# Optimization experiments

Hardware: AMD Instinct MI355X
Metric: run time of the kernel (lower is better)

The kernel has to match this reference:

```python
import jax, jax.numpy as jnp
import numpy as np

F, N, C, H, M = 256, 400, 128, 8, 128  # frames, batch*joints, mdl_channels, heads, max_pos
E = C // H


def _layer_norm(z, g, b, eps=1e-5):
    mu = jnp.mean(z, axis=-1, keepdims=True)
    var = jnp.mean((z - mu) ** 2, axis=-1, keepdims=True)
    return (z - mu) * jax.lax.rsqrt(var + eps) * g + b


def setup_inputs() -> dict:
    key = jax.random.key(0)
    ks = jax.random.split(key, 16)
    s = 0.02
    return {
        "x": jax.random.normal(ks[0], (F, N, C), jnp.float32),
        "tree_encoding": jax.random.normal(ks[1], (N, C), jnp.float32),
        "W_qkv": jax.random.normal(ks[2], (3 * C, C), jnp.float32) * s,      # Linear weight (out,in), no bias
        "W_tree_k": jax.random.normal(ks[3], (C, C), jnp.float32) * s,
        "W_tree_v": jax.random.normal(ks[4], (C, C), jnp.float32) * s,
        "emb": jax.random.normal(ks[5], (2 * M + 1, E), jnp.float32) * s,    # distance embedding table
        "W_beta": jax.random.normal(ks[6], (1, 3 * C), jnp.float32) * s,     # lin_beta (out,in), no bias
        "ln1_g": jnp.ones((C,), jnp.float32),
        "ln1_b": jnp.zeros((C,), jnp.float32),
        "ln2_g": jnp.ones((C,), jnp.float32),
        "ln2_b": jnp.zeros((C,), jnp.float32),
        "W1": jax.random.normal(ks[7], (C, C), jnp.float32) * s,
        "b1": jnp.zeros((C,), jnp.float32),
        "W2": jax.random.normal(ks[8], (C, C), jnp.float32) * s,
        "b2": jnp.zeros((C,), jnp.float32),
    }


def reference(x, tree_encoding, W_qkv, W_tree_k, W_tree_v, emb, W_beta,
              ln1_g, ln1_b, ln2_g, ln2_b, W1, b1, W2, b2):
    f, n, c = x.shape
    # qkv projection, no bias
    qkv = x @ W_qkv.T                          # (f, n, 3c)
    q, k, v = jnp.split(qkv, 3, axis=-1)       # each (f, n, c)
    # tree positional encoding added to key/value
    k = k + (tree_encoding @ W_tree_k)[None]
    v = v + (tree_encoding @ W_tree_v)[None]
    # (f, n, c) -> (n, f, h, e): n is the attention batch, f is sequence length
    to_heads = lambda t: t.transpose(1, 0, 2).reshape(n, f, H, E)
    qh, kh, vh = to_heads(q), to_heads(k), to_heads(v)
    # content scores
    qk = jnp.einsum('nlhe,nshe->nhls', qh, kh)
    # relative position bias
    ids = jnp.arange(f)
    dist = jnp.clip(ids[:, None] - ids[None, :], -M, M) + M   # (f, f)
    pe = emb[dist]                                            # (f, f, e)
    qk = qk + jnp.einsum('nlhe,lse->nhls', qh, pe)
    qk = qk + jnp.einsum('nshe,lse->nhls', kh, pe)
    scale = 1.0 / (E ** 0.5)
    att = jax.nn.softmax(qk * scale, axis=-1)                 # (n, h, f, f)
    out = jnp.einsum('nhls,nshe->nlhe', att, vh)              # (n, f, h, e)
    y = out.reshape(n, f, c).transpose(1, 0, 2)               # (f, n, c)
    # gated AddNorm (beta=True): x is residual, y is attention output
    gate = jax.nn.sigmoid(jnp.concatenate([y, x, y - x], axis=-1) @ W_beta.T)
    h1 = _layer_norm(gate * x + (1.0 - gate) * y, ln1_g, ln1_b)
    # FFN (GELU exact, as torch nn.GELU default)
    ff = jax.nn.gelu(h1 @ W1.T + b1, approximate=False) @ W2.T + b2
    return _layer_norm(ff + h1, ln2_g, ln2_b)
```

## Files before the change

kernel.cpp:

```cpp
#include <hip/hip_runtime.h>
#include <math.h>

#define F_DIM 256
#define N_DIM 400
#define C_DIM 128
#define H_DIM 8
#define E_DIM 16
#define ROWS  (F_DIM * N_DIM)
#define SBUF  (N_DIM * H_DIM * F_DIM * E_DIM)

#define S_SCALE 0.6005612043932249f

typedef _Float16 half2_t __attribute__((ext_vector_type(2)));
typedef _Float16 f16x8   __attribute__((ext_vector_type(8)));
typedef float    f32x16  __attribute__((ext_vector_type(16)));
typedef float    f32x4   __attribute__((ext_vector_type(4)));

struct H2x4 { half2_t h[4]; };

__device__ inline f16x8 pack8(float4 a, float4 b) {
    H2x4 t;
    t.h[0] = __builtin_bit_cast(half2_t, __builtin_amdgcn_cvt_pkrtz(a.x, a.y));
    t.h[1] = __builtin_bit_cast(half2_t, __builtin_amdgcn_cvt_pkrtz(a.z, a.w));
    t.h[2] = __builtin_bit_cast(half2_t, __builtin_amdgcn_cvt_pkrtz(b.x, b.y));
    t.h[3] = __builtin_bit_cast(half2_t, __builtin_amdgcn_cvt_pkrtz(b.z, b.w));
    return __builtin_bit_cast(f16x8, t);
}

__device__ inline _Float16 h_rtz(float v) {
    half2_t p = __builtin_bit_cast(half2_t, __builtin_amdgcn_cvt_pkrtz(v, v));
    return p[0];
}

__device__ inline int iclamp256(int v) { return v < 0 ? 0 : (v > 256 ? 256 : v); }

__global__ __launch_bounds__(256) void prep_pack(
    const float* __restrict__ x, const float* __restrict__ Wq,
    const float* __restrict__ emb, const float* __restrict__ te,
    const float* __restrict__ Wtk, const float* __restrict__ Wtv,
    _Float16* __restrict__ xh, _Float16* __restrict__ Wqh,
    _Float16* __restrict__ embh, float* __restrict__ tk, float* __restrict__ tv)
{
    int bid = blockIdx.x;
    int t   = threadIdx.x;
    if (bid < 6400) {
        int i = (bid * 256 + t) * 8;
        const float4* s = (const float4*)(x + i);
        *(uint4*)(xh + i) = __builtin_bit_cast(uint4, pack8(s[0], s[1]));
    } else if (bid < 6424) {
        int i = ((bid - 6400) * 256 + t) * 8;
        const float4* s = (const float4*)(Wq + i);
        *(uint4*)(Wqh + i) = __builtin_bit_cast(uint4, pack8(s[0], s[1]));
    } else if (bid < 6426) {
        int r = (bid - 6424) * 256 + t;
        if (r > 256) return;
        const float4* er = (const float4*)(emb + r * 16);
        float4 e0 = er[0], e1 = er[1], e2 = er[2], e3 = er[3];
        e0.x *= S_SCALE; e0.y *= S_SCALE; e0.z *= S_SCALE; e0.w *= S_SCALE;
        e1.x *= S_SCALE; e1.y *= S_SCALE; e1.z *= S_SCALE; e1.w *= S_SCALE;
        e2.x *= S_SCALE; e2.y *= S_SCALE; e2.z *= S_SCALE; e2.w *= S_SCALE;
        e3.x *= S_SCALE; e3.y *= S_SCALE; e3.z *= S_SCALE; e3.w *= S_SCALE;
        *(uint4*)(embh + r * 16)     = __builtin_bit_cast(uint4, pack8(e0, e1));
        *(uint4*)(embh + r * 16 + 8) = __builtin_bit_cast(uint4, pack8(e2, e3));
    } else {
        int n = bid - 6426;
        const float* W = (t < 128) ? Wtk : Wtv;
        float* outp    = (t < 128) ? tk : tv;
        int j = t & 127;
        float acc = 0.f;
        #pragma unroll 4
        for (int c = 0; c < 128; ++c)
            acc += te[n * 128 + c] * W[c * 128 + j];
        outp[n * 128 + j] = acc;
    }
}

__global__ __launch_bounds__(256) void qkv_gemm(
    const _Float16* __restrict__ xh, const _Float16* __restrict__ Wqh,
    const float* __restrict__ tk, const float* __restrict__ tv,
    _Float16* __restrict__ qn, _Float16* __restrict__ kn, _Float16* __restrict__ vn)
{
    int tid  = threadIdx.x;
    int wave = tid >> 6, lane = tid & 63;
    int m32  = lane & 31, khalf = lane >> 5;

    int bid = blockIdx.x;
    int xcd = bid & 7;
    int tt  = bid >> 3;
    int cb  = tt % 6;
    int rp  = (tt / 6) * 8 + xcd;
    int row0 = rp * 64 + (wave & 1) * 32;
    int col0 = cb * 64 + (wave >> 1) * 32;

    const _Float16* xp = xh  + (row0 + m32) * 128 + khalf * 8;
    const _Float16* wp = Wqh + (col0 + m32) * 128 + khalf * 8;

    f32x16 acc;
    #pragma unroll
    for (int i = 0; i < 16; ++i) acc[i] = 0.f;

    #pragma unroll
    for (int k0 = 0; k0 < 128; k0 += 16) {
        f16x8 xa = __builtin_bit_cast(f16x8, *(const uint4*)(xp + k0));
        f16x8 wa = __builtin_bit_cast(f16x8, *(const uint4*)(wp + k0));
        acc = __builtin_amdgcn_mfma_f32_32x32x16_f16(xa, wa, acc, 0, 0, 0);
    }

    int o   = col0 + m32;
    int sec = o >> 7;
    int rem = o & 127;
    #pragma unroll
    for (int reg = 0; reg < 16; ++reg) {
        int r = row0 + (reg & 3) + 8 * (reg >> 2) + 4 * khalf;
        float val = acc[reg];
        if (sec == 0) {
            qn[r * 128 + rem] = h_rtz(val * S_SCALE);
        } else {
            int f = r / 400;
            int n = r - f * 400;
            if (sec == 1) {
                kn[r * 128 + rem] = h_rtz((val + tk[n * 128 + rem]) * S_SCALE);
            } else {
                vn[r * 128 + rem] = (_Float16)(val + tv[n * 128 + rem]);
            }
        }
    }
}

__global__ __launch_bounds__(256) void v_pack(
    const _Float16* __restrict__ vn, _Float16* __restrict__ vT)
{
    __shared__ _Float16 sm[16 * 264];
    int bn = blockIdx.x;
    int n  = bn >> 3, h = bn & 7;
    int t  = threadIdx.x;

    const uint4* src = (const uint4*)(vn + (t * 400 + n) * 128 + h * 16);
    uint4 a = src[0], b = src[1];
    union { uint4 u; _Float16 hv[8]; } ua, ub;
    ua.u = a; ub.u = b;
    #pragma unroll
    for (int e = 0; e < 8; ++e) sm[e * 264 + t]       = ua.hv[e];
    #pragma unroll
    for (int e = 0; e < 8; ++e) sm[(e + 8) * 264 + t] = ub.hv[e];
    __syncthreads();

    #pragma unroll
    for (int k = 0; k < 2; ++k) {
        int idx = (k * 256 + t) * 8;
        int e = idx >> 8, f0 = idx & 255;
        uint4 o = *(const uint4*)(sm + e * 264 + f0);
        *(uint4*)(vT + bn * 4096 + idx) = o;
    }
}

#define R2_STRIDE 258
#define PS_STRIDE 40

__global__ __launch_bounds__(512, 4) void attn_kernel(
    const _Float16* __restrict__ qb, const _Float16* __restrict__ kb,
    const _Float16* __restrict__ vb, const _Float16* __restrict__ embh,
    _Float16* __restrict__ y)
{
    __shared__ __align__(16) _Float16 R2sh[32 * R2_STRIDE];
    __shared__ __align__(16) _Float16 Psh[8 * 32 * PS_STRIDE];

    int tid  = threadIdx.x;
    int wave = tid >> 6, lane = tid & 63;
    int bid  = blockIdx.x;
    int bn   = (bid & 7) * 400 + (bid >> 3);
    int n    = bn >> 3, h = bn & 7;
    int base = bn * 4096;

    int nn  = lane & 31;
    int kh  = lane >> 5;
    int khb = (lane & 32) << 2;
    int cbase = 31 + 4 * kh - nn;
    int dbase = 4 * kh - nn;
    int q16 = (lane >> 4) & 3;

    int nat_off = n * 128 + h * 16 + kh * 8;

    f16x8 aq = __builtin_bit_cast(f16x8,
        *(const uint4*)(qb + (32 * wave + nn) * 51200 + nat_off));

    f16x8 bones;
    #pragma unroll
    for (int i = 0; i < 8; ++i) bones[i] = (_Float16)1.0f;

    f32x4 O[2];
    f32x4 Od[2];
    #pragma unroll
    for (int a = 0; a < 2; ++a)
        #pragma unroll
        for (int r = 0; r < 4; ++r) { O[a][r] = 0.f; Od[a][r] = 0.f; }

    _Float16* psw = Psh + wave * 32 * PS_STRIDE;

    for (int st = 0; st < 8; ++st) {
        f16x8 bk = __builtin_bit_cast(f16x8,
            *(const uint4*)(kb + (32 * st + nn) * 51200 + nat_off));

        auto r2tile = [&](int ct) {
            int erow = 32 * ct + nn; if (erow > 256) erow = 256;
            f16x8 be = __builtin_bit_cast(f16x8,
                *(const uint4*)(embh + erow * 16 + kh * 8));
            f32x16 c2;
            #pragma unroll
            for (int i = 0; i < 16; ++i) c2[i] = 0.f;
            c2 = __builtin_amdgcn_mfma_f32_32x32x16_f16(bk, be, c2, 0, 0, 0);
            int col = 32 * ct + nn;
            if (col <= 256) {
                #pragma unroll
                for (int r = 0; r < 16; ++r) {
                    int srow = (r & 3) + 8 * (r >> 2) + 4 * kh;
                    R2sh[srow * R2_STRIDE + col] = (_Float16)c2[r];
                }
            }
        };
        r2tile(wave);
        if (wave == (st & 7)) r2tile(8);
        __syncthreads();

        f16x8 bv = __builtin_bit_cast(f16x8,
            *(const uint4*)(vb + base + (lane & 15) * 256 + 32 * st + q16 * 8));

        int U0 = 32 * wave - 32 * st + 128;

        f32x16 S;
        #pragma unroll
        for (int i = 0; i < 16; ++i) S[i] = 0.f;
        S = __builtin_amdgcn_mfma_f32_32x32x16_f16(aq, bk, S, 0, 0, 0);

        int br0 = iclamp256(U0 - 31 + nn);
        int br1 = iclamp256(U0 + 1 + nn);
        f16x8 be0 = __builtin_bit_cast(f16x8,
            *(const uint4*)(embh + br0 * 16 + kh * 8));
        f16x8 be1 = __builtin_bit_cast(f16x8,
            *(const uint4*)(embh + br1 * 16 + kh * 8));
        f32x16 W0, W1;
        #pragma unroll
        for (int i = 0; i < 16; ++i) { W0[i] = 0.f; W1[i] = 0.f; }
        W0 = __builtin_amdgcn_mfma_f32_32x32x16_f16(aq, be0, W0, 0, 0, 0);
        W1 = __builtin_amdgcn_mfma_f32_32x32x16_f16(aq, be1, W1, 0, 0, 0);

        half2_t b1p[8];
        #pragma unroll
        for (int r = 0; r < 16; ++r) {
            int rmr = (r & 3) + 8 * (r >> 2);
            int c   = rmr + cbase;
            int addr = ((c & 31) << 2) + khb;
            int w01 = __builtin_bit_cast(int,
                __builtin_amdgcn_cvt_pkrtz(W0[r], W1[r]));
            half2_t hh = __builtin_bit_cast(half2_t,
                __builtin_amdgcn_ds_bpermute(addr, w01));
            b1p[r >> 1][r & 1] = (c < 32) ? hh[0] : hh[1];
        }

        #pragma unroll
        for (int r = 0; r < 16; ++r) {
            int rmr = (r & 3) + 8 * (r >> 2);
            float b1 = (float)b1p[r >> 1][r & 1];
            int d = iclamp256(U0 + rmr + dbase);
            float b2 = (float)R2sh[nn * R2_STRIDE + d];
            float p = __builtin_amdgcn_exp2f(S[r] + b1 + b2);
            int mloc = rmr + 4 * kh;
            psw[mloc * PS_STRIDE + nn] = (_Float16)p;
        }

        #pragma unroll
        for (int a = 0; a < 2; ++a) {
            f16x8 ap = __builtin_bit_cast(f16x8,
                *(const uint4*)(psw + (16 * a + (lane & 15)) * PS_STRIDE + q16 * 8));
            O[a]  = __builtin_amdgcn_mfma_f32_16x16x32_f16(ap, bv,    O[a],  0, 0, 0);
            Od[a] = __builtin_amdgcn_mfma_f32_16x16x32_f16(ap, bones, Od[a], 0, 0, 0);
        }
        __syncthreads();
    }

    #pragma unroll
    for (int a = 0; a < 2; ++a) {
        #pragma unroll
        for (int r = 0; r < 4; ++r) {
            int row  = q16 * 4 + r;
            int lloc = 16 * a + row;
            int lg = 32 * wave + lloc;
            y[(lg * 400 + n) * 128 + h * 16 + (lane & 15)] =
                (_Float16)(O[a][r] / Od[a][r]);
        }
    }
}

__global__ __launch_bounds__(256) void gate_ln1(
    const float* __restrict__ x, const _Float16* __restrict__ yh,
    const float* __restrict__ Wb, const float* __restrict__ g,
    const float* __restrict__ b, float* __restrict__ h1,
    _Float16* __restrict__ h1h)
{
    int tid  = threadIdx.x;
    int r    = blockIdx.x * 4 + (tid >> 6);
    int lane = tid & 63;
    int c    = lane * 2;

    float2 xv = *(const float2*)(x + r * 128 + c);
    half2_t yv2 = *(const half2_t*)(yh + r * 128 + c);
    float yvx = (float)yv2[0], yvy = (float)yv2[1];
    float2 w0 = *(const float2*)(Wb + c);
    float2 w1 = *(const float2*)(Wb + 128 + c);
    float2 w2 = *(const float2*)(Wb + 256 + c);

    float sv = yvx * w0.x + yvy * w0.y
             + xv.x * w1.x + xv.y * w1.y
             + (yvx - xv.x) * w2.x + (yvy - xv.y) * w2.y;
    #pragma unroll
    for (int off = 32; off > 0; off >>= 1) sv += __shfl_xor(sv, off);
    float gate = 1.0f / (1.0f + __expf(-sv));

    float z0 = gate * xv.x + (1.0f - gate) * yvx;
    float z1 = gate * xv.y + (1.0f - gate) * yvy;
    float s1 = z0 + z1, s2 = z0 * z0 + z1 * z1;
    #pragma unroll
    for (int off = 32; off > 0; off >>= 1) {
        s1 += __shfl_xor(s1, off);
        s2 += __shfl_xor(s2, off);
    }
    float mu  = s1 * (1.0f / 128.0f);
    float var = s2 * (1.0f / 128.0f) - mu * mu;
    float rs  = rsqrtf(var + 1e-5f);

    float2 gv = *(const float2*)(g + c);
    float2 bv = *(const float2*)(b + c);
    float2 ov;
    ov.x = (z0 - mu) * rs * gv.x + bv.x;
    ov.y = (z1 - mu) * rs * gv.y + bv.y;
    *(float2*)(h1 + r * 128 + c) = ov;
    *(uint*)(h1h + r * 128 + c) = __builtin_bit_cast(uint,
        __builtin_amdgcn_cvt_pkrtz(ov.x, ov.y));
}

__global__ __launch_bounds__(256) void ff1_gemm(
    const _Float16* __restrict__ A, const float* __restrict__ W,
    const float* __restrict__ bias, _Float16* __restrict__ outp)
{
    int tid  = threadIdx.x;
    int wave = tid >> 6, lane = tid & 63;
    int m32  = lane & 31, khalf = lane >> 5;

    int bid = blockIdx.x;
    int xcd = bid & 7;
    int tt  = bid >> 3;
    int cb  = tt & 1;
    int rp  = (tt >> 1) * 8 + xcd;
    int row0 = rp * 64 + (wave & 1) * 32;
    int col0 = cb * 64 + (wave >> 1) * 32;

    const _Float16* ap = A + (row0 + m32) * 128 + khalf * 8;
    const float*    wp = W + (col0 + m32) * 128 + khalf * 8;

    f32x16 acc;
    #pragma unroll
    for (int i = 0; i < 16; ++i) acc[i] = 0.f;

    #pragma unroll
    for (int k0 = 0; k0 < 128; k0 += 16) {
        f16x8 aa16 = __builtin_bit_cast(f16x8, *(const uint4*)(ap + k0));
        float4 wa = *(const float4*)(wp + k0);
        float4 wb = *(const float4*)(wp + k0 + 4);
        acc = __builtin_amdgcn_mfma_f32_32x32x16_f16(aa16, pack8(wa, wb), acc, 0, 0, 0);
    }

    int   c  = col0 + m32;
    float bi = bias[c];
    #pragma unroll
    for (int reg = 0; reg < 16; ++reg) {
        int r = row0 + (reg & 3) + 8 * (reg >> 2) + 4 * khalf;
        float v = acc[reg] + bi;
        v = 0.5f * v * (1.0f + erff(v * 0.70710678118654752f));
        outp[r * 128 + c] = (_Float16)v;
    }
}

__global__ __launch_bounds__(256) void ff2_ln2(
    const _Float16* __restrict__ A, const float* __restrict__ W2,
    const float* __restrict__ b2, const float* __restrict__ h1,
    const float* __restrict__ g, const float* __restrict__ bb,
    float* __restrict__ outp)
{
    __shared__ float Cs[32 * 132];
    int tid  = threadIdx.x;
    int wave = tid >> 6, lane = tid & 63;
    int m32  = lane & 31, khalf = lane >> 5;
    int row0 = blockIdx.x * 32;
    int col0 = wave * 32;

    const _Float16* ap = A  + (row0 + m32) * 128 + khalf * 8;
    const float*    wp = W2 + (col0 + m32) * 128 + khalf * 8;

    f32x16 acc;
    #pragma unroll
    for (int i = 0; i < 16; ++i) acc[i] = 0.f;

    #pragma unroll
    for (int k0 = 0; k0 < 128; k0 += 16) {
        f16x8 aa16 = __builtin_bit_cast(f16x8, *(const uint4*)(ap + k0));
        float4 wa = *(const float4*)(wp + k0);
        float4 wb = *(const float4*)(wp + k0 + 4);
        acc = __builtin_amdgcn_mfma_f32_32x32x16_f16(aa16, pack8(wa, wb), acc, 0, 0, 0);
    }

    #pragma unroll
    for (int reg = 0; reg < 16; ++reg) {
        int rloc = (reg & 3) + 8 * (reg >> 2) + 4 * khalf;
        Cs[rloc * 132 + col0 + m32] = acc[reg];
    }
    __syncthreads();

    int rloc = tid >> 3, seg = (tid & 7) * 16;
    int r = row0 + rloc;
    float z[16];
    float s1 = 0.f, s2 = 0.f;
    #pragma unroll
    for (int j4 = 0; j4 < 4; ++j4) {
        float4 cv = *(const float4*)(Cs + rloc * 132 + seg + j4 * 4);
        float4 hv = *(const float4*)(h1 + r * 128 + seg + j4 * 4);
        float4 bv = *(const float4*)(b2 + seg + j4 * 4);
        z[j4*4+0] = cv.x + bv.x + hv.x;
        z[j4*4+1] = cv.y + bv.y + hv.y;
        z[j4*4+2] = cv.z + bv.z + hv.z;
        z[j4*4+3] = cv.w + bv.w + hv.w;
        s1 += z[j4*4+0] + z[j4*4+1] + z[j4*4+2] + z[j4*4+3];
        s2 += z[j4*4+0]*z[j4*4+0] + z[j4*4+1]*z[j4*4+1]
            + z[j4*4+2]*z[j4*4+2] + z[j4*4+3]*z[j4*4+3];
    }
    #pragma unroll
    for (int off = 4; off > 0; off >>= 1) {
        s1 += __shfl_xor(s1, off);
        s2 += __shfl_xor(s2, off);
    }
    float mu  = s1 * (1.0f / 128.0f);
    float var = s2 * (1.0f / 128.0f) - mu * mu;
    float rs  = rsqrtf(var + 1e-5f);
    #pragma unroll
    for (int j4 = 0; j4 < 4; ++j4) {
        float4 gv = *(const float4*)(g  + seg + j4 * 4);
        float4 bv = *(const float4*)(bb + seg + j4 * 4);
        float4 ov;
        ov.x = (z[j4*4+0] - mu) * rs * gv.x + bv.x;
        ov.y = (z[j4*4+1] - mu) * rs * gv.y + bv.y;
        ov.z = (z[j4*4+2] - mu) * rs * gv.z + bv.z;
        ov.w = (z[j4*4+3] - mu) * rs * gv.w + bv.w;
        *(float4*)(outp + r * 128 + seg + j4 * 4) = ov;
    }
}

extern "C" void kernel_launch(void* const* d_in, const int* in_sizes, int n_in,
                              void* d_out, int out_size, void* d_ws, size_t ws_size,
                              hipStream_t stream)
{
    const float* x     = (const float*)d_in[0];
    const float* te    = (const float*)d_in[1];
    const float* Wqkv  = (const float*)d_in[2];
    const float* Wtk   = (const float*)d_in[3];
    const float* Wtv   = (const float*)d_in[4];
    const float* emb   = (const float*)d_in[5];
    const float* Wbeta = (const float*)d_in[6];
    const float* ln1g  = (const float*)d_in[7];
    const float* ln1b  = (const float*)d_in[8];
    const float* ln2g  = (const float*)d_in[9];
    const float* ln2b  = (const float*)d_in[10];
    const float* W1    = (const float*)d_in[11];
    const float* b1    = (const float*)d_in[12];
    const float* W2    = (const float*)d_in[13];
    const float* b2    = (const float*)d_in[14];
    float* outp = (float*)d_out;

    float* ws = (float*)d_ws;
    float* tk = ws;
    float* tv = ws + 51200;
    float* qb_region = ws + 102400;
    float* kb_region = qb_region + SBUF;
    float* vb_region = kb_region + SBUF;
    float* yb        = vb_region + SBUF;

    _Float16* qnat = (_Float16*)qb_region;
    _Float16* knat = (_Float16*)kb_region;
    _Float16* vnat = (_Float16*)vb_region;
    _Float16* vT   = (_Float16*)(vb_region + SBUF / 2);
    _Float16* embh = (_Float16*)(qb_region + SBUF / 2);
    _Float16* yh   = (_Float16*)yb;
    _Float16* xh   = (_Float16*)(kb_region + SBUF / 2);
    _Float16* Wqh  = (_Float16*)(yb + SBUF / 2);

    float*    h1   = kb_region;
    _Float16* h1h  = (_Float16*)vb_region;
    _Float16* ff1h = (_Float16*)qb_region;

    prep_pack<<<6826, 256, 0, stream>>>(x, Wqkv, emb, te, Wtk, Wtv,
                                        xh, Wqh, embh, tk, tv);
    qkv_gemm<<<9600, 256, 0, stream>>>(xh, Wqh, tk, tv, qnat, knat, vnat);
    v_pack<<<3200, 256, 0, stream>>>(vnat, vT);
    attn_kernel<<<3200, 512, 0, stream>>>(qnat, knat, vT, embh, yh);
    gate_ln1<<<ROWS / 4, 256, 0, stream>>>(x, yh, Wbeta, ln1g, ln1b, h1, h1h);
    ff1_gemm<<<3200, 256, 0, stream>>>(h1h, W1, b1, ff1h);
    ff2_ln2<<<3200, 256, 0, stream>>>(ff1h, W2, b2, h1, ln2g, ln2b, outp);
}
```

Baseline: 519.2 us.

## Fuse gated AddNorm, FFN GEMMs and second LayerNorm into one kernel

Combines the gate+LN1, FF1+GELU and FF2+LN2 kernels into a single kernel per 32-row tile. The LN1 output and GELU activations are kept in shared memory and registers instead of being written to and re-read from global workspace, and two kernel launches are removed. Each block now does all stages serially, adding LDS usage and barriers; the XCD-aware block remapping of the old FF1 kernel is dropped.

```diff
diff --git a/kernel.cpp b/kernel.cpp
--- a/kernel.cpp
+++ b/kernel.cpp
@@ -291,36 +291,67 @@
     }
 }
 
-__global__ __launch_bounds__(256) void gate_ln1(
+__global__ __launch_bounds__(256) void ffn_fused(
     const float* __restrict__ x, const _Float16* __restrict__ yh,
-    const float* __restrict__ Wb, const float* __restrict__ g,
-    const float* __restrict__ b, float* __restrict__ h1,
-    _Float16* __restrict__ h1h)
+    const float* __restrict__ Wb,
+    const float* __restrict__ ln1g, const float* __restrict__ ln1b,
+    const float* __restrict__ W1, const float* __restrict__ b1,
+    const float* __restrict__ W2, const float* __restrict__ b2,
+    const float* __restrict__ ln2g, const float* __restrict__ ln2b,
+    float* __restrict__ outp)
 {
+    __shared__ __align__(16) _Float16 h1sh[32 * 136];
+    __shared__ __align__(16) _Float16 gsh[32 * 136];
+    __shared__ float Cs[32 * 132];
+
     int tid  = threadIdx.x;
-    int r    = blockIdx.x * 4 + (tid >> 6);
-    int lane = tid & 63;
-    int c    = lane * 2;
-
-    float2 xv = *(const float2*)(x + r * 128 + c);
-    half2_t yv2 = *(const half2_t*)(yh + r * 128 + c);
-    float yvx = (float)yv2[0], yvy = (float)yv2[1];
-    float2 w0 = *(const float2*)(Wb + c);
-    float2 w1 = *(const float2*)(Wb + 128 + c);
-    float2 w2 = *(const float2*)(Wb + 256 + c);
-
-    float sv = yvx * w0.x + yvy * w0.y
-             + xv.x * w1.x + xv.y * w1.y
-             + (yvx - xv.x) * w2.x + (yvy - xv.y) * w2.y;
-    #pragma unroll
-    for (int off = 32; off > 0; off >>= 1) sv += __shfl_xor(sv, off);
+    int rloc = tid >> 3;
+    int seg  = (tid & 7) * 16;
+    int r    = blockIdx.x * 32 + rloc;
+
+    float xv[16], yv[16];
+    {
+        const float4* xp = (const float4*)(x + r * 128 + seg);
+        float4 x0 = xp[0], x1 = xp[1], x2 = xp[2], x3 = xp[3];
+        xv[0]=x0.x; xv[1]=x0.y; xv[2]=x0.z; xv[3]=x0.w;
+        xv[4]=x1.x; xv[5]=x1.y; xv[6]=x1.z; xv[7]=x1.w;
+        xv[8]=x2.x; xv[9]=x2.y; xv[10]=x2.z; xv[11]=x2.w;
+        xv[12]=x3.x; xv[13]=x3.y; xv[14]=x3.z; xv[15]=x3.w;
+        const uint4* yp = (const uint4*)(yh + r * 128 + seg);
+        uint4 y0 = yp[0], y1 = yp[1];
+        union { uint4 u; _Float16 hv[8]; } uy0, uy1;
+        uy0.u = y0; uy1.u = y1;
+        #pragma unroll
+        for (int j = 0; j < 8; ++j) { yv[j] = (float)uy0.hv[j]; yv[8+j] = (float)uy1.hv[j]; }
+    }
+    float sv = 0.f;
+    {
+        const float4* w0p = (const float4*)(Wb + seg);
+        const float4* w1p = (const float4*)(Wb + 128 + seg);
+        const float4* w2p = (const float4*)(Wb + 256 + seg);
+        #pragma unroll
+        for (int j4 = 0; j4 < 4; ++j4) {
+            float4 w0 = w0p[j4], w1 = w1p[j4], w2 = w2p[j4];
+            float* w0f = (float*)&w0; float* w1f = (float*)&w1; float* w2f = (float*)&w2;
+            #pragma unroll
+            for (int jj = 0; jj < 4; ++jj) {
+                int j = j4 * 4 + jj;
+                sv += yv[j] * w0f[jj] + xv[j] * w1f[jj] + (yv[j] - xv[j]) * w2f[jj];
+            }
+        }
+    }
+    #pragma unroll
+    for (int off = 4; off > 0; off >>= 1) sv += __shfl_xor(sv, off);
     float gate = 1.0f / (1.0f + __expf(-sv));
 
-    float z0 = gate * xv.x + (1.0f - gate) * yvx;
-    float z1 = gate * xv.y + (1.0f - gate) * yvy;
-    float s1 = z0 + z1, s2 = z0 * z0 + z1 * z1;
-    #pragma unroll
-    for (int off = 32; off > 0; off >>= 1) {
+    float z[16], s1 = 0.f, s2 = 0.f;
+    #pragma unroll
+    for (int j = 0; j < 16; ++j) {
+        z[j] = gate * xv[j] + (1.0f - gate) * yv[j];
+        s1 += z[j]; s2 += z[j] * z[j];
+    }
+    #pragma unroll
+    for (int off = 4; off > 0; off >>= 1) {
         s1 += __shfl_xor(s1, off);
         s2 += __shfl_xor(s2, off);
     }
@@ -328,127 +359,111 @@
     float var = s2 * (1.0f / 128.0f) - mu * mu;
     float rs  = rsqrtf(var + 1e-5f);
 
-    float2 gv = *(const float2*)(g + c);
-    float2 bv = *(const float2*)(b + c);
-    float2 ov;
-    ov.x = (z0 - mu) * rs * gv.x + bv.x;
-    ov.y = (z1 - mu) * rs * gv.y + bv.y;
-    *(float2*)(h1 + r * 128 + c) = ov;
-    *(uint*)(h1h + r * 128 + c) = __builtin_bit_cast(uint,
-        __builtin_amdgcn_cvt_pkrtz(ov.x, ov.y));
-}
-
-__global__ __launch_bounds__(256) void ff1_gemm(
-    const _Float16* __restrict__ A, const float* __restrict__ W,
-    const float* __restrict__ bias, _Float16* __restrict__ outp)
-{
-    int tid  = threadIdx.x;
+    float h1r[16];
+    {
+        const float4* gp = (const float4*)(ln1g + seg);
+        const float4* bp = (const float4*)(ln1b + seg);
+        #pragma unroll
+        for (int j4 = 0; j4 < 4; ++j4) {
+            float4 gv = gp[j4], bv = bp[j4];
+            float* gf = (float*)&gv; float* bf = (float*)&bv;
+            #pragma unroll
+            for (int jj = 0; jj < 4; ++jj) {
+                int j = j4 * 4 + jj;
+                h1r[j] = (z[j] - mu) * rs * gf[jj] + bf[jj];
+            }
+        }
+        #pragma unroll
+        for (int j = 0; j < 8; ++j) {
+            *(uint*)(h1sh + rloc * 136 + seg + 2 * j) = __builtin_bit_cast(uint,
+                __builtin_amdgcn_cvt_pkrtz(h1r[2 * j], h1r[2 * j + 1]));
+        }
+    }
+    __syncthreads();
+
     int wave = tid >> 6, lane = tid & 63;
     int m32  = lane & 31, khalf = lane >> 5;
-
-    int bid = blockIdx.x;
-    int xcd = bid & 7;
-    int tt  = bid >> 3;
-    int cb  = tt & 1;
-    int rp  = (tt >> 1) * 8 + xcd;
-    int row0 = rp * 64 + (wave & 1) * 32;
-    int col0 = cb * 64 + (wave >> 1) * 32;
-
-    const _Float16* ap = A + (row0 + m32) * 128 + khalf * 8;
-    const float*    wp = W + (col0 + m32) * 128 + khalf * 8;
-
-    f32x16 acc;
-    #pragma unroll
-    for (int i = 0; i < 16; ++i) acc[i] = 0.f;
-
-    #pragma unroll
-    for (int k0 = 0; k0 < 128; k0 += 16) {
-        f16x8 aa16 = __builtin_bit_cast(f16x8, *(const uint4*)(ap + k0));
-        float4 wa = *(const float4*)(wp + k0);
-        float4 wb = *(const float4*)(wp + k0 + 4);
-        acc = __builtin_amdgcn_mfma_f32_32x32x16_f16(aa16, pack8(wa, wb), acc, 0, 0, 0);
-    }
-
-    int   c  = col0 + m32;
-    float bi = bias[c];
-    #pragma unroll
-    for (int reg = 0; reg < 16; ++reg) {
-        int r = row0 + (reg & 3) + 8 * (reg >> 2) + 4 * khalf;
-        float v = acc[reg] + bi;
-        v = 0.5f * v * (1.0f + erff(v * 0.70710678118654752f));
-        outp[r * 128 + c] = (_Float16)v;
-    }
-}
-
-__global__ __launch_bounds__(256) void ff2_ln2(
-    const _Float16* __restrict__ A, const float* __restrict__ W2,
-    const float* __restrict__ b2, const float* __restrict__ h1,
-    const float* __restrict__ g, const float* __restrict__ bb,
-    float* __restrict__ outp)
-{
-    __shared__ float Cs[32 * 132];
-    int tid  = threadIdx.x;
-    int wave = tid >> 6, lane = tid & 63;
-    int m32  = lane & 31, khalf = lane >> 5;
-    int row0 = blockIdx.x * 32;
     int col0 = wave * 32;
-
-    const _Float16* ap = A  + (row0 + m32) * 128 + khalf * 8;
-    const float*    wp = W2 + (col0 + m32) * 128 + khalf * 8;
-
-    f32x16 acc;
-    #pragma unroll
-    for (int i = 0; i < 16; ++i) acc[i] = 0.f;
-
-    #pragma unroll
-    for (int k0 = 0; k0 < 128; k0 += 16) {
-        f16x8 aa16 = __builtin_bit_cast(f16x8, *(const uint4*)(ap + k0));
-        float4 wa = *(const float4*)(wp + k0);
-        float4 wb = *(const float4*)(wp + k0 + 4);
-        acc = __builtin_amdgcn_mfma_f32_32x32x16_f16(aa16, pack8(wa, wb), acc, 0, 0, 0);
-    }
-
-    #pragma unroll
-    for (int reg = 0; reg < 16; ++reg) {
-        int rloc = (reg & 3) + 8 * (reg >> 2) + 4 * khalf;
-        Cs[rloc * 132 + col0 + m32] = acc[reg];
+    {
+        f32x16 acc;
+        #pragma unroll
+        for (int i = 0; i < 16; ++i) acc[i] = 0.f;
+        const _Float16* ap = h1sh + m32 * 136 + khalf * 8;
+        const float*    wp = W1 + (col0 + m32) * 128 + khalf * 8;
+        #pragma unroll
+        for (int k0 = 0; k0 < 128; k0 += 16) {
+            f16x8 aa = __builtin_bit_cast(f16x8, *(const uint4*)(ap + k0));
+            float4 wa = *(const float4*)(wp + k0);
+            float4 wb = *(const float4*)(wp + k0 + 4);
+            acc = __builtin_amdgcn_mfma_f32_32x32x16_f16(aa, pack8(wa, wb), acc, 0, 0, 0);
+        }
+        int   c  = col0 + m32;
+        float bi = b1[c];
+        #pragma unroll
+        for (int reg = 0; reg < 16; ++reg) {
+            int row2 = (reg & 3) + 8 * (reg >> 2) + 4 * khalf;
+            float v = acc[reg] + bi;
+            v = 0.5f * v * (1.0f + erff(v * 0.70710678118654752f));
+            gsh[row2 * 136 + c] = (_Float16)v;
+        }
     }
     __syncthreads();
 
-    int rloc = tid >> 3, seg = (tid & 7) * 16;
-    int r = row0 + rloc;
-    float z[16];
-    float s1 = 0.f, s2 = 0.f;
+    {
+        f32x16 acc;
+        #pragma unroll
+        for (int i = 0; i < 16; ++i) acc[i] = 0.f;
+        const _Float16* ap = gsh + m32 * 136 + khalf * 8;
+        const float*    wp = W2 + (col0 + m32) * 128 + khalf * 8;
+        #pragma unroll
+        for (int k0 = 0; k0 < 128; k0 += 16) {
+            f16x8 aa = __builtin_bit_cast(f16x8, *(const uint4*)(ap + k0));
+            float4 wa = *(const float4*)(wp + k0);
+            float4 wb = *(const float4*)(wp + k0 + 4);
+            acc = __builtin_amdgcn_mfma_f32_32x32x16_f16(aa, pack8(wa, wb), acc, 0, 0, 0);
+        }
+        #pragma unroll
+        for (int reg = 0; reg < 16; ++reg) {
+            int row2 = (reg & 3) + 8 * (reg >> 2) + 4 * khalf;
+            Cs[row2 * 132 + col0 + m32] = acc[reg];
+        }
+    }
+    __syncthreads();
+
+    float z2[16];
+    float t1 = 0.f, t2 = 0.f;
     #pragma unroll
     for (int j4 = 0; j4 < 4; ++j4) {
         float4 cv = *(const float4*)(Cs + rloc * 132 + seg + j4 * 4);
-        float4 hv = *(const float4*)(h1 + r * 128 + seg + j4 * 4);
         float4 bv = *(const float4*)(b2 + seg + j4 * 4);
-        z[j4*4+0] = cv.x + bv.x + hv.x;
-        z[j4*4+1] = cv.y + bv.y + hv.y;
-        z[j4*4+2] = cv.z + bv.z + hv.z;
-        z[j4*4+3] = cv.w + bv.w + hv.w;
-        s1 += z[j4*4+0] + z[j4*4+1] + z[j4*4+2] + z[j4*4+3];
-        s2 += z[j4*4+0]*z[j4*4+0] + z[j4*4+1]*z[j4*4+1]
-            + z[j4*4+2]*z[j4*4+2] + z[j4*4+3]*z[j4*4+3];
+        float* cf = (float*)&cv; float* bf = (float*)&bv;
+        #pragma unroll
+        for (int jj = 0; jj < 4; ++jj) {
+            int j = j4 * 4 + jj;
+            z2[j] = cf[jj] + bf[jj] + h1r[j];
+            t1 += z2[j]; t2 += z2[j] * z2[j];
+        }
     }
     #pragma unroll
     for (int off = 4; off > 0; off >>= 1) {
-        s1 += __shfl_xor(s1, off);
-        s2 += __shfl_xor(s2, off);
-    }
-    float mu  = s1 * (1.0f / 128.0f);
-    float var = s2 * (1.0f / 128.0f) - mu * mu;
-    float rs  = rsqrtf(var + 1e-5f);
+        t1 += __shfl_xor(t1, off);
+        t2 += __shfl_xor(t2, off);
+    }
+    float mu2  = t1 * (1.0f / 128.0f);
+    float var2 = t2 * (1.0f / 128.0f) - mu2 * mu2;
+    float rs2  = rsqrtf(var2 + 1e-5f);
     #pragma unroll
     for (int j4 = 0; j4 < 4; ++j4) {
-        float4 gv = *(const float4*)(g  + seg + j4 * 4);
-        float4 bv = *(const float4*)(bb + seg + j4 * 4);
+        float4 gv = *(const float4*)(ln2g + seg + j4 * 4);
+        float4 bv = *(const float4*)(ln2b + seg + j4 * 4);
+        float* gf = (float*)&gv; float* bf = (float*)&bv;
         float4 ov;
-        ov.x = (z[j4*4+0] - mu) * rs * gv.x + bv.x;
-        ov.y = (z[j4*4+1] - mu) * rs * gv.y + bv.y;
-        ov.z = (z[j4*4+2] - mu) * rs * gv.z + bv.z;
-        ov.w = (z[j4*4+3] - mu) * rs * gv.w + bv.w;
+        float* of = (float*)&ov;
+        #pragma unroll
+        for (int jj = 0; jj < 4; ++jj) {
+            int j = j4 * 4 + jj;
+            of[jj] = (z2[j] - mu2) * rs2 * gf[jj] + bf[jj];
+        }
         *(float4*)(outp + r * 128 + seg + j4 * 4) = ov;
     }
 }
@@ -491,16 +506,11 @@
     _Float16* xh   = (_Float16*)(kb_region + SBUF / 2);
     _Float16* Wqh  = (_Float16*)(yb + SBUF / 2);
 
-    float*    h1   = kb_region;
-    _Float16* h1h  = (_Float16*)vb_region;
-    _Float16* ff1h = (_Float16*)qb_region;
-
     prep_pack<<<6826, 256, 0, stream>>>(x, Wqkv, emb, te, Wtk, Wtv,
                                         xh, Wqh, embh, tk, tv);
     qkv_gemm<<<9600, 256, 0, stream>>>(xh, Wqh, tk, tv, qnat, knat, vnat);
     v_pack<<<3200, 256, 0, stream>>>(vnat, vT);
     attn_kernel<<<3200, 512, 0, stream>>>(qnat, knat, vT, embh, yh);
-    gate_ln1<<<ROWS / 4, 256, 0, stream>>>(x, yh, Wbeta, ln1g, ln1b, h1, h1h);
-    ff1_gemm<<<3200, 256, 0, stream>>>(h1h, W1, b1, ff1h);
-    ff2_ln2<<<3200, 256, 0, stream>>>(ff1h, W2, b2, h1, ln2g, ln2b, outp);
-}
+    ffn_fused<<<3200, 256, 0, stream>>>(x, yh, Wbeta, ln1g, ln1b,
+                                        W1, b1, W2, b2, ln2g, ln2b, outp);
+}
```

New measurement: 479.9 us. 7.6% less time.
